# Kernel tuning notes

Measured on AMD Instinct MI355X. Metric: run time of the kernel, lower is better.

## Reference

```python
import jax, jax.numpy as jnp
import numpy as np

B, N, IN_DIM, OUT_DIM = 8, 2048, 128, 128
NEG_SLOPE = 0.2

def setup_inputs() -> dict:
    key = jax.random.key(0)
    k1, k2, k3, k4 = jax.random.split(key, 4)
    x = jax.random.normal(k1, (B, N, IN_DIM), dtype=jnp.float32)
    adj = jax.random.randint(k2, (N, N), 0, 2, dtype=jnp.int32)
    # nn.Linear weight init scale ~ 1/sqrt(fan_in)
    W = jax.random.normal(k3, (IN_DIM, OUT_DIM), dtype=jnp.float32) / np.sqrt(IN_DIM)
    a_vec = jax.random.normal(k4, (2 * OUT_DIM,), dtype=jnp.float32) / np.sqrt(2 * OUT_DIM)
    return {"x": x, "adj": adj, "W": W, "a_vec": a_vec}

def reference(x, adj, W, a_vec):
    # h = x @ W : [b, n, d]
    h = jnp.einsum("bni,io->bno", x, W)
    # Algebraic decomposition of a([h_i, h_j]) = a1.h_i + a2.h_j
    a1, a2 = a_vec[:OUT_DIM], a_vec[OUT_DIM:]
    s_i = h @ a1  # [b, n] score contribution from source node i
    s_j = h @ a2  # [b, n] score contribution from target node j
    e = s_i[:, :, None] + s_j[:, None, :]  # [b, n, n]
    e = jnp.where(e >= 0, e, NEG_SLOPE * e)  # leaky_relu(0.2)
    mask = (adj > 0)[None, :, :]  # [1, n, n] broadcast over batch
    e = jnp.where(mask, e, -jnp.inf)
    alpha = jax.nn.softmax(e, axis=-1)  # [b, n, n]
    out = jnp.einsum("bnm,bmd->bnd", alpha, h)  # [b, n, d]
    return out, alpha
```

## Files before the change

kernel.cpp:

```cpp
#include <hip/hip_runtime.h>
#include <hip/hip_bf16.h>
#include <cstdint>
#include <cstddef>

constexpr int Bn = 8;
constexpr int Nn = 2048;
constexpr int Dn = 128;

typedef __bf16 bf16x8 __attribute__((ext_vector_type(8)));
typedef float f32x4 __attribute__((ext_vector_type(4)));

__global__ __launch_bounds__(256) void gat_k1(
    const float* __restrict__ x, const float* __restrict__ W,
    const float* __restrict__ a_vec,
    __bf16* __restrict__ hT, float* __restrict__ s1, float* __restrict__ s2) {
  __shared__ __align__(16) float Wl[64 * 144];
  __shared__ __align__(16) float xL[32 * 132];

  const int t = threadIdx.x;
  const int r0 = blockIdx.x * 32;
  const int b = r0 >> 11;
  const int n0 = r0 & (Nn - 1);
  const int rp = (t >> 4) << 1;
  const int c0 = (t & 15) << 3;
  const int c0p = c0 + ((c0 >> 5) << 2);

  float acc[2][8];
#pragma unroll
  for (int r = 0; r < 2; ++r)
#pragma unroll
    for (int c = 0; c < 8; ++c) acc[r][c] = 0.f;

#pragma unroll
  for (int it = 0; it < 4; ++it) {
    int idx = t + (it << 8);
    int rr = idx >> 5, kc = (idx & 31) << 2;
    *(float4*)(xL + rr * 132 + kc) = *(const float4*)(x + (size_t)(r0 + rr) * Dn + kc);
  }

  for (int ph = 0; ph < 2; ++ph) {
    if (ph) __syncthreads();
#pragma unroll
    for (int it = 0; it < 8; ++it) {
      int idx = t + (it << 8);
      int kk = idx >> 5, c4 = (idx & 31) << 2;
      int dsto = kk * 144 + c4 + ((c4 >> 5) << 2);
      *(float4*)(Wl + dsto) = *(const float4*)(W + (size_t)((ph << 6) + kk) * Dn + c4);
    }
    __syncthreads();
    const float* xrow = xL + rp * 132 + (ph << 6);
    for (int k = 0; k < 64; ++k) {
      float xa0 = xrow[k];
      float xa1 = xrow[132 + k];
      float4 w0 = *(const float4*)(Wl + k * 144 + c0p);
      float4 w1 = *(const float4*)(Wl + k * 144 + c0p + 4);
      float ws[8] = {w0.x, w0.y, w0.z, w0.w, w1.x, w1.y, w1.z, w1.w};
#pragma unroll
      for (int c = 0; c < 8; ++c) {
        acc[0][c] = fmaf(xa0, ws[c], acc[0][c]);
        acc[1][c] = fmaf(xa1, ws[c], acc[1][c]);
      }
    }
  }

  float q1[2] = {0.f, 0.f}, q2[2] = {0.f, 0.f};
#pragma unroll
  for (int c = 0; c < 8; ++c) {
    float a1c = a_vec[c0 + c];
    float a2c = a_vec[Dn + c0 + c];
    q1[0] = fmaf(acc[0][c], a1c, q1[0]);
    q1[1] = fmaf(acc[1][c], a1c, q1[1]);
    q2[0] = fmaf(acc[0][c], a2c, q2[0]);
    q2[1] = fmaf(acc[1][c], a2c, q2[1]);
  }
#pragma unroll
  for (int d = 1; d < 16; d <<= 1) {
    q1[0] += __shfl_xor(q1[0], d);
    q1[1] += __shfl_xor(q1[1], d);
    q2[0] += __shfl_xor(q2[0], d);
    q2[1] += __shfl_xor(q2[1], d);
  }
  if ((t & 15) == 0) {
    s1[b * Nn + n0 + rp] = q1[0];
    s1[b * Nn + n0 + rp + 1] = q1[1];
    s2[b * Nn + n0 + rp] = q2[0];
    s2[b * Nn + n0 + rp + 1] = q2[1];
  }

#pragma unroll
  for (int c = 0; c < 8; ++c) {
    union { __bf16 h[2]; uint32_t u; } pk;
    pk.h[0] = (__bf16)acc[0][c];
    pk.h[1] = (__bf16)acc[1][c];
    *(uint32_t*)(hT + (size_t)(b * Dn + c0 + c) * Nn + n0 + rp) = pk.u;
  }
}

__global__ __launch_bounds__(512) void gat_k2(
    const int* __restrict__ adj, const __bf16* __restrict__ hT,
    const float* __restrict__ s1, const float* __restrict__ s2,
    float* __restrict__ out, float* __restrict__ alpha) {
  __shared__ __align__(16) float sj[Nn];
  __shared__ float siv[32], invl[32];
  __shared__ __align__(16) __bf16 Pl[2][32 * 72];

  const int t = threadIdx.x;
  const int b = blockIdx.x >> 6;
  const int i0 = (blockIdx.x & 63) << 5;
  const int w = t >> 6, lane = t & 63;
  const int ii = t >> 4, sub = t & 15;
  const int q16 = lane >> 4, m16 = lane & 15;
  const int d0 = w << 4;
  const __bf16* __restrict__ hTb = hT + (size_t)b * Dn * Nn;

  *(float4*)(sj + (t << 2)) = *(const float4*)(s2 + b * Nn + (t << 2));
  if (t < 32) siv[t] = s1[b * Nn + i0 + t];
  __syncthreads();

  const int i = i0 + ii;
  const int* __restrict__ adjrow = adj + (size_t)i * Nn;
  const float si = siv[ii];

  float l = 0.f;
  uint32_t mb0 = 0, mb1 = 0, mb2 = 0, mb3 = 0;
#define PASS1_G(G, MW)                                                        \
  {                                                                           \
    _Pragma("unroll")                                                         \
    for (int u = 0; u < 8; ++u) {                                             \
      int j = (((G) << 3) + u) * 64 + (sub << 2);                             \
      int4 am = *(const int4*)(adjrow + j);                                   \
      float4 sv = *(const float4*)(sj + j);                                   \
      float e0 = si + sv.x; e0 = fmaxf(e0, 0.2f * e0);                        \
      float e1 = si + sv.y; e1 = fmaxf(e1, 0.2f * e1);                        \
      float e2 = si + sv.z; e2 = fmaxf(e2, 0.2f * e2);                        \
      float e3 = si + sv.w; e3 = fmaxf(e3, 0.2f * e3);                        \
      l += (am.x > 0) ? __expf(e0) : 0.f;                                     \
      l += (am.y > 0) ? __expf(e1) : 0.f;                                     \
      l += (am.z > 0) ? __expf(e2) : 0.f;                                     \
      l += (am.w > 0) ? __expf(e3) : 0.f;                                     \
      uint32_t mbt = (am.x > 0 ? 1u : 0u) | (am.y > 0 ? 2u : 0u) |            \
                     (am.z > 0 ? 4u : 0u) | (am.w > 0 ? 8u : 0u);             \
      MW |= mbt << (u << 2);                                                  \
    }                                                                         \
  }
  PASS1_G(0, mb0)
  PASS1_G(1, mb1)
  PASS1_G(2, mb2)
  PASS1_G(3, mb3)
#undef PASS1_G

  l += __shfl_xor(l, 1);
  l += __shfl_xor(l, 2);
  l += __shfl_xor(l, 4);
  l += __shfl_xor(l, 8);
  if (sub == 0) invl[ii] = 1.f / l;
  __syncthreads();
  const float il = invl[ii];

  f32x4 acc0 = {0.f, 0.f, 0.f, 0.f}, acc1 = {0.f, 0.f, 0.f, 0.f};
  float* __restrict__ arow = alpha + ((size_t)(b * Nn + i) << 11);

  const __bf16* __restrict__ bp = hTb + (size_t)(d0 + m16) * Nn + (q16 << 3);

  auto alpha_phase = [&](int k) {
    int j = (k << 6) + (sub << 2);
    float4 sv = *(const float4*)(sj + j);
    uint32_t mw = (k & 16) ? ((k & 8) ? mb3 : mb2) : ((k & 8) ? mb1 : mb0);
    int sh = (k & 7) << 2;
    float e0 = si + sv.x; e0 = fmaxf(e0, 0.2f * e0);
    float e1 = si + sv.y; e1 = fmaxf(e1, 0.2f * e1);
    float e2 = si + sv.z; e2 = fmaxf(e2, 0.2f * e2);
    float e3 = si + sv.w; e3 = fmaxf(e3, 0.2f * e3);
    float a0 = ((mw >> (sh + 0)) & 1u) ? __expf(e0) * il : 0.f;
    float a1 = ((mw >> (sh + 1)) & 1u) ? __expf(e1) * il : 0.f;
    float a2 = ((mw >> (sh + 2)) & 1u) ? __expf(e2) * il : 0.f;
    float a3 = ((mw >> (sh + 3)) & 1u) ? __expf(e3) * il : 0.f;
    f32x4 av = {a0, a1, a2, a3};
    __builtin_nontemporal_store(av, (f32x4*)(arow + j));
    union { __bf16 h[4]; uint2 u2; } pk;
    pk.h[0] = (__bf16)a0; pk.h[1] = (__bf16)a1;
    pk.h[2] = (__bf16)a2; pk.h[3] = (__bf16)a3;
    *(uint2*)(&Pl[k & 1][ii * 72 + (sub << 2)]) = pk.u2;
  };

  auto mfma_win = [&](int k, bf16x8 bc0, bf16x8 bc1) {
    const __bf16* plb = Pl[k & 1];
    bf16x8 a00 = *(const bf16x8*)(plb + m16 * 72 + (q16 << 3));
    bf16x8 a01 = *(const bf16x8*)(plb + m16 * 72 + 32 + (q16 << 3));
    bf16x8 a10 = *(const bf16x8*)(plb + (16 + m16) * 72 + (q16 << 3));
    bf16x8 a11 = *(const bf16x8*)(plb + (16 + m16) * 72 + 32 + (q16 << 3));
    acc0 = __builtin_amdgcn_mfma_f32_16x16x32_bf16(a00, bc0, acc0, 0, 0, 0);
    acc0 = __builtin_amdgcn_mfma_f32_16x16x32_bf16(a01, bc1, acc0, 0, 0, 0);
    acc1 = __builtin_amdgcn_mfma_f32_16x16x32_bf16(a10, bc0, acc1, 0, 0, 0);
    acc1 = __builtin_amdgcn_mfma_f32_16x16x32_bf16(a11, bc1, acc1, 0, 0, 0);
  };

  bf16x8 c0 = *(const bf16x8*)(bp);
  bf16x8 c1 = *(const bf16x8*)(bp + 32);
  alpha_phase(0);
  asm volatile("s_waitcnt lgkmcnt(0)\n\ts_barrier" ::: "memory");

#pragma unroll
  for (int jt = 0; jt < 31; ++jt) {
    bf16x8 n0 = *(const bf16x8*)(bp + ((jt + 1) << 6));
    bf16x8 n1 = *(const bf16x8*)(bp + ((jt + 1) << 6) + 32);
    __builtin_amdgcn_sched_barrier(0);
    mfma_win(jt, c0, c1);
    alpha_phase(jt + 1);
    asm volatile("s_waitcnt lgkmcnt(0)\n\ts_barrier" ::: "memory");
    c0 = n0; c1 = n1;
  }
  mfma_win(31, c0, c1);

#pragma unroll
  for (int ib = 0; ib < 2; ++ib) {
    f32x4 a = ib ? acc1 : acc0;
    int d = d0 + m16;
#pragma unroll
    for (int r = 0; r < 4; ++r) {
      int irow = i0 + (ib << 4) + (q16 << 2) + r;
      out[((size_t)(b * Nn + irow) << 7) + d] = a[r];
    }
  }
}

extern "C" void kernel_launch(void* const* d_in, const int* in_sizes, int n_in,
                              void* d_out, int out_size, void* d_ws, size_t ws_size,
                              hipStream_t stream) {
  const float* x = (const float*)d_in[0];
  const int* adj = (const int*)d_in[1];
  const float* W = (const float*)d_in[2];
  const float* a_vec = (const float*)d_in[3];

  float* out = (float*)d_out;
  float* alpha = out + (size_t)Bn * Nn * Dn;

  char* ws = (char*)d_ws;
  __bf16* hT = (__bf16*)ws;
  float* s1 = (float*)(ws + (size_t)Bn * Dn * Nn * 2);
  float* s2 = s1 + (size_t)Bn * Nn;

  gat_k1<<<512, 256, 0, stream>>>(x, W, a_vec, hT, s1, s2);
  gat_k2<<<512, 512, 0, stream>>>(adj, hT, s1, s2, out, alpha);
}
```

Before: 196.3 us.

## Halve rows per block in GAT attention kernel, widen j-tile, swizzle LDS

The attention kernel now handles 16 query rows per block instead of 32 and launches 1024 blocks, with 32 threads per row covering 128-column tiles over 16 steps instead of 64-column tiles over 32. The P tile in LDS now uses an XOR swizzle in place of padding, each wave issues four MFMAs per tile on a single accumulator, and the launch bounds request higher occupancy. The aim is more blocks in flight and fewer barrier steps to hide memory latency on the large alpha writes. In exchange, the hT B-operand loads are no longer prefetched one tile ahead, and each block reloads the full hT slice for half as many rows, doubling hT reads.

```diff
diff --git a/kernel.cpp b/kernel.cpp
--- a/kernel.cpp
+++ b/kernel.cpp
@@ -96,76 +96,71 @@
   }
 }
 
-__global__ __launch_bounds__(512) void gat_k2(
+__global__ __launch_bounds__(512, 8) void gat_k2(
     const int* __restrict__ adj, const __bf16* __restrict__ hT,
     const float* __restrict__ s1, const float* __restrict__ s2,
     float* __restrict__ out, float* __restrict__ alpha) {
   __shared__ __align__(16) float sj[Nn];
-  __shared__ float siv[32], invl[32];
-  __shared__ __align__(16) __bf16 Pl[2][32 * 72];
+  __shared__ float siv[16], invl[16];
+  __shared__ __align__(16) __bf16 Pl[2][16 * 128];
 
   const int t = threadIdx.x;
-  const int b = blockIdx.x >> 6;
-  const int i0 = (blockIdx.x & 63) << 5;
+  const int b = blockIdx.x >> 7;
+  const int i0 = (blockIdx.x & 127) << 4;
   const int w = t >> 6, lane = t & 63;
-  const int ii = t >> 4, sub = t & 15;
+  const int row = t >> 5;
+  const int jl = (t & 31) << 2;
   const int q16 = lane >> 4, m16 = lane & 15;
   const int d0 = w << 4;
   const __bf16* __restrict__ hTb = hT + (size_t)b * Dn * Nn;
 
   *(float4*)(sj + (t << 2)) = *(const float4*)(s2 + b * Nn + (t << 2));
-  if (t < 32) siv[t] = s1[b * Nn + i0 + t];
+  if (t < 16) siv[t] = s1[b * Nn + i0 + t];
   __syncthreads();
 
-  const int i = i0 + ii;
+  const int i = i0 + row;
   const int* __restrict__ adjrow = adj + (size_t)i * Nn;
-  const float si = siv[ii];
+  const float si = siv[row];
 
   float l = 0.f;
-  uint32_t mb0 = 0, mb1 = 0, mb2 = 0, mb3 = 0;
-#define PASS1_G(G, MW)                                                        \
-  {                                                                           \
-    _Pragma("unroll")                                                         \
-    for (int u = 0; u < 8; ++u) {                                             \
-      int j = (((G) << 3) + u) * 64 + (sub << 2);                             \
-      int4 am = *(const int4*)(adjrow + j);                                   \
-      float4 sv = *(const float4*)(sj + j);                                   \
-      float e0 = si + sv.x; e0 = fmaxf(e0, 0.2f * e0);                        \
-      float e1 = si + sv.y; e1 = fmaxf(e1, 0.2f * e1);                        \
-      float e2 = si + sv.z; e2 = fmaxf(e2, 0.2f * e2);                        \
-      float e3 = si + sv.w; e3 = fmaxf(e3, 0.2f * e3);                        \
-      l += (am.x > 0) ? __expf(e0) : 0.f;                                     \
-      l += (am.y > 0) ? __expf(e1) : 0.f;                                     \
-      l += (am.z > 0) ? __expf(e2) : 0.f;                                     \
-      l += (am.w > 0) ? __expf(e3) : 0.f;                                     \
-      uint32_t mbt = (am.x > 0 ? 1u : 0u) | (am.y > 0 ? 2u : 0u) |            \
-                     (am.z > 0 ? 4u : 0u) | (am.w > 0 ? 8u : 0u);             \
-      MW |= mbt << (u << 2);                                                  \
-    }                                                                         \
-  }
-  PASS1_G(0, mb0)
-  PASS1_G(1, mb1)
-  PASS1_G(2, mb2)
-  PASS1_G(3, mb3)
-#undef PASS1_G
-
+  uint32_t mb0 = 0, mb1 = 0;
+#pragma unroll
+  for (int k = 0; k < 16; ++k) {
+    int j = (k << 7) + jl;
+    int4 am = *(const int4*)(adjrow + j);
+    float4 sv = *(const float4*)(sj + j);
+    float e0 = si + sv.x; e0 = fmaxf(e0, 0.2f * e0);
+    float e1 = si + sv.y; e1 = fmaxf(e1, 0.2f * e1);
+    float e2 = si + sv.z; e2 = fmaxf(e2, 0.2f * e2);
+    float e3 = si + sv.w; e3 = fmaxf(e3, 0.2f * e3);
+    l += (am.x > 0) ? __expf(e0) : 0.f;
+    l += (am.y > 0) ? __expf(e1) : 0.f;
+    l += (am.z > 0) ? __expf(e2) : 0.f;
+    l += (am.w > 0) ? __expf(e3) : 0.f;
+    uint32_t mbt = (am.x > 0 ? 1u : 0u) | (am.y > 0 ? 2u : 0u) |
+                   (am.z > 0 ? 4u : 0u) | (am.w > 0 ? 8u : 0u);
+    if (k < 8) mb0 |= mbt << (k << 2);
+    else       mb1 |= mbt << ((k & 7) << 2);
+  }
   l += __shfl_xor(l, 1);
   l += __shfl_xor(l, 2);
   l += __shfl_xor(l, 4);
   l += __shfl_xor(l, 8);
-  if (sub == 0) invl[ii] = 1.f / l;
+  l += __shfl_xor(l, 16);
+  if ((t & 31) == 0) invl[row] = 1.f / l;
   __syncthreads();
-  const float il = invl[ii];
-
-  f32x4 acc0 = {0.f, 0.f, 0.f, 0.f}, acc1 = {0.f, 0.f, 0.f, 0.f};
+  const float il = invl[row];
+
+  f32x4 acc = {0.f, 0.f, 0.f, 0.f};
   float* __restrict__ arow = alpha + ((size_t)(b * Nn + i) << 11);
 
   const __bf16* __restrict__ bp = hTb + (size_t)(d0 + m16) * Nn + (q16 << 3);
+  const int swz = (m16 & 7) << 4;
 
   auto alpha_phase = [&](int k) {
-    int j = (k << 6) + (sub << 2);
+    int j = (k << 7) + jl;
     float4 sv = *(const float4*)(sj + j);
-    uint32_t mw = (k & 16) ? ((k & 8) ? mb3 : mb2) : ((k & 8) ? mb1 : mb0);
+    uint32_t mw = (k & 8) ? mb1 : mb0;
     int sh = (k & 7) << 2;
     float e0 = si + sv.x; e0 = fmaxf(e0, 0.2f * e0);
     float e1 = si + sv.y; e1 = fmaxf(e1, 0.2f * e1);
@@ -180,47 +175,44 @@
     union { __bf16 h[4]; uint2 u2; } pk;
     pk.h[0] = (__bf16)a0; pk.h[1] = (__bf16)a1;
     pk.h[2] = (__bf16)a2; pk.h[3] = (__bf16)a3;
-    *(uint2*)(&Pl[k & 1][ii * 72 + (sub << 2)]) = pk.u2;
+    *(uint2*)((char*)(&Pl[k & 1][0]) + (row << 8) +
+              (((jl << 1)) ^ ((row & 7) << 4))) = pk.u2;
   };
 
-  auto mfma_win = [&](int k, bf16x8 bc0, bf16x8 bc1) {
-    const __bf16* plb = Pl[k & 1];
-    bf16x8 a00 = *(const bf16x8*)(plb + m16 * 72 + (q16 << 3));
-    bf16x8 a01 = *(const bf16x8*)(plb + m16 * 72 + 32 + (q16 << 3));
-    bf16x8 a10 = *(const bf16x8*)(plb + (16 + m16) * 72 + (q16 << 3));
-    bf16x8 a11 = *(const bf16x8*)(plb + (16 + m16) * 72 + 32 + (q16 << 3));
-    acc0 = __builtin_amdgcn_mfma_f32_16x16x32_bf16(a00, bc0, acc0, 0, 0, 0);
-    acc0 = __builtin_amdgcn_mfma_f32_16x16x32_bf16(a01, bc1, acc0, 0, 0, 0);
-    acc1 = __builtin_amdgcn_mfma_f32_16x16x32_bf16(a10, bc0, acc1, 0, 0, 0);
-    acc1 = __builtin_amdgcn_mfma_f32_16x16x32_bf16(a11, bc1, acc1, 0, 0, 0);
+  auto mfma_win = [&](int parity, bf16x8 c0, bf16x8 c1, bf16x8 c2, bf16x8 c3) {
+    const char* plb = (const char*)(&Pl[parity][0]) + (m16 << 8);
+    bf16x8 a0 = *(const bf16x8*)(plb + (((0 << 6) + (q16 << 4)) ^ swz));
+    bf16x8 a1 = *(const bf16x8*)(plb + (((1 << 6) + (q16 << 4)) ^ swz));
+    bf16x8 a2 = *(const bf16x8*)(plb + (((2 << 6) + (q16 << 4)) ^ swz));
+    bf16x8 a3 = *(const bf16x8*)(plb + (((3 << 6) + (q16 << 4)) ^ swz));
+    acc = __builtin_amdgcn_mfma_f32_16x16x32_bf16(a0, c0, acc, 0, 0, 0);
+    acc = __builtin_amdgcn_mfma_f32_16x16x32_bf16(a1, c1, acc, 0, 0, 0);
+    acc = __builtin_amdgcn_mfma_f32_16x16x32_bf16(a2, c2, acc, 0, 0, 0);
+    acc = __builtin_amdgcn_mfma_f32_16x16x32_bf16(a3, c3, acc, 0, 0, 0);
   };
 
-  bf16x8 c0 = *(const bf16x8*)(bp);
-  bf16x8 c1 = *(const bf16x8*)(bp + 32);
   alpha_phase(0);
   asm volatile("s_waitcnt lgkmcnt(0)\n\ts_barrier" ::: "memory");
 
 #pragma unroll
-  for (int jt = 0; jt < 31; ++jt) {
-    bf16x8 n0 = *(const bf16x8*)(bp + ((jt + 1) << 6));
-    bf16x8 n1 = *(const bf16x8*)(bp + ((jt + 1) << 6) + 32);
+  for (int jt = 0; jt < 16; ++jt) {
+    const __bf16* cp = bp + (jt << 7);
+    bf16x8 c0 = *(const bf16x8*)(cp);
+    bf16x8 c1 = *(const bf16x8*)(cp + 32);
+    bf16x8 c2 = *(const bf16x8*)(cp + 64);
+    bf16x8 c3 = *(const bf16x8*)(cp + 96);
     __builtin_amdgcn_sched_barrier(0);
-    mfma_win(jt, c0, c1);
-    alpha_phase(jt + 1);
-    asm volatile("s_waitcnt lgkmcnt(0)\n\ts_barrier" ::: "memory");
-    c0 = n0; c1 = n1;
-  }
-  mfma_win(31, c0, c1);
-
-#pragma unroll
-  for (int ib = 0; ib < 2; ++ib) {
-    f32x4 a = ib ? acc1 : acc0;
-    int d = d0 + m16;
-#pragma unroll
-    for (int r = 0; r < 4; ++r) {
-      int irow = i0 + (ib << 4) + (q16 << 2) + r;
-      out[((size_t)(b * Nn + irow) << 7) + d] = a[r];
-    }
+    if (jt < 15) alpha_phase(jt + 1);
+    mfma_win(jt & 1, c0, c1, c2, c3);
+    if (jt < 15)
+      asm volatile("s_waitcnt lgkmcnt(0)\n\ts_barrier" ::: "memory");
+  }
+
+  int d = d0 + m16;
+#pragma unroll
+  for (int r = 0; r < 4; ++r) {
+    int irow = i0 + (q16 << 2) + r;
+    out[((size_t)(b * Nn + irow) << 7) + d] = acc[r];
   }
 }
 
@@ -241,5 +233,5 @@
   float* s2 = s1 + (size_t)Bn * Nn;
 
   gat_k1<<<512, 256, 0, stream>>>(x, W, a_vec, hT, s1, s2);
-  gat_k2<<<512, 512, 0, stream>>>(adj, hT, s1, s2, out, alpha);
+  gat_k2<<<1024, 512, 0, stream>>>(adj, hT, s1, s2, out, alpha);
 }
```

Result: slower. 232.0 us (+18.2%).

## Split fused softmax+aggregation kernel into separate alpha and matmul kernels

Applied to the files above, without the earlier changes.

Replaces the fused kernel, which computed alpha and fed it to MFMA through LDS with per-tile barriers, with two kernels. The first computes the masked softmax and writes alpha. The second reads alpha back from global memory as fp32, converts it to bf16 and does the alpha·h matmul with MFMA. This removes the barrier-heavy interleaving and the LDS staging, but adds a full re-read of the 128 MB alpha tensor plus an extra launch.

```diff
diff --git a/kernel.cpp b/kernel.cpp
--- a/kernel.cpp
+++ b/kernel.cpp
@@ -96,30 +96,25 @@
   }
 }
 
-__global__ __launch_bounds__(512) void gat_k2(
-    const int* __restrict__ adj, const __bf16* __restrict__ hT,
-    const float* __restrict__ s1, const float* __restrict__ s2,
-    float* __restrict__ out, float* __restrict__ alpha) {
+__global__ __launch_bounds__(256) void gat_kA(
+    const int* __restrict__ adj, const float* __restrict__ s1,
+    const float* __restrict__ s2, float* __restrict__ alpha) {
   __shared__ __align__(16) float sj[Nn];
-  __shared__ float siv[32], invl[32];
-  __shared__ __align__(16) __bf16 Pl[2][32 * 72];
+  __shared__ float siv[16];
 
   const int t = threadIdx.x;
-  const int b = blockIdx.x >> 6;
-  const int i0 = (blockIdx.x & 63) << 5;
-  const int w = t >> 6, lane = t & 63;
-  const int ii = t >> 4, sub = t & 15;
-  const int q16 = lane >> 4, m16 = lane & 15;
-  const int d0 = w << 4;
-  const __bf16* __restrict__ hTb = hT + (size_t)b * Dn * Nn;
-
-  *(float4*)(sj + (t << 2)) = *(const float4*)(s2 + b * Nn + (t << 2));
-  if (t < 32) siv[t] = s1[b * Nn + i0 + t];
+  const int b = blockIdx.x >> 7;
+  const int i0 = (blockIdx.x & 127) << 4;
+  const int row = t >> 4, sub = t & 15;
+
+  *(float4*)(sj + (t << 3)) = *(const float4*)(s2 + b * Nn + (t << 3));
+  *(float4*)(sj + (t << 3) + 4) = *(const float4*)(s2 + b * Nn + (t << 3) + 4);
+  if (t < 16) siv[t] = s1[b * Nn + i0 + t];
   __syncthreads();
 
-  const int i = i0 + ii;
+  const int i = i0 + row;
   const int* __restrict__ adjrow = adj + (size_t)i * Nn;
-  const float si = siv[ii];
+  const float si = siv[row];
 
   float l = 0.f;
   uint32_t mb0 = 0, mb1 = 0, mb2 = 0, mb3 = 0;
@@ -153,16 +148,12 @@
   l += __shfl_xor(l, 2);
   l += __shfl_xor(l, 4);
   l += __shfl_xor(l, 8);
-  if (sub == 0) invl[ii] = 1.f / l;
-  __syncthreads();
-  const float il = invl[ii];
-
-  f32x4 acc0 = {0.f, 0.f, 0.f, 0.f}, acc1 = {0.f, 0.f, 0.f, 0.f};
+  const float il = 1.f / l;
+
   float* __restrict__ arow = alpha + ((size_t)(b * Nn + i) << 11);
 
-  const __bf16* __restrict__ bp = hTb + (size_t)(d0 + m16) * Nn + (q16 << 3);
-
-  auto alpha_phase = [&](int k) {
+#pragma unroll
+  for (int k = 0; k < 32; ++k) {
     int j = (k << 6) + (sub << 2);
     float4 sv = *(const float4*)(sj + j);
     uint32_t mw = (k & 16) ? ((k & 8) ? mb3 : mb2) : ((k & 8) ? mb1 : mb0);
@@ -177,49 +168,58 @@
     float a3 = ((mw >> (sh + 3)) & 1u) ? __expf(e3) * il : 0.f;
     f32x4 av = {a0, a1, a2, a3};
     __builtin_nontemporal_store(av, (f32x4*)(arow + j));
-    union { __bf16 h[4]; uint2 u2; } pk;
-    pk.h[0] = (__bf16)a0; pk.h[1] = (__bf16)a1;
-    pk.h[2] = (__bf16)a2; pk.h[3] = (__bf16)a3;
-    *(uint2*)(&Pl[k & 1][ii * 72 + (sub << 2)]) = pk.u2;
-  };
-
-  auto mfma_win = [&](int k, bf16x8 bc0, bf16x8 bc1) {
-    const __bf16* plb = Pl[k & 1];
-    bf16x8 a00 = *(const bf16x8*)(plb + m16 * 72 + (q16 << 3));
-    bf16x8 a01 = *(const bf16x8*)(plb + m16 * 72 + 32 + (q16 << 3));
-    bf16x8 a10 = *(const bf16x8*)(plb + (16 + m16) * 72 + (q16 << 3));
-    bf16x8 a11 = *(const bf16x8*)(plb + (16 + m16) * 72 + 32 + (q16 << 3));
-    acc0 = __builtin_amdgcn_mfma_f32_16x16x32_bf16(a00, bc0, acc0, 0, 0, 0);
-    acc0 = __builtin_amdgcn_mfma_f32_16x16x32_bf16(a01, bc1, acc0, 0, 0, 0);
-    acc1 = __builtin_amdgcn_mfma_f32_16x16x32_bf16(a10, bc0, acc1, 0, 0, 0);
-    acc1 = __builtin_amdgcn_mfma_f32_16x16x32_bf16(a11, bc1, acc1, 0, 0, 0);
-  };
-
-  bf16x8 c0 = *(const bf16x8*)(bp);
-  bf16x8 c1 = *(const bf16x8*)(bp + 32);
-  alpha_phase(0);
-  asm volatile("s_waitcnt lgkmcnt(0)\n\ts_barrier" ::: "memory");
-
-#pragma unroll
-  for (int jt = 0; jt < 31; ++jt) {
-    bf16x8 n0 = *(const bf16x8*)(bp + ((jt + 1) << 6));
-    bf16x8 n1 = *(const bf16x8*)(bp + ((jt + 1) << 6) + 32);
-    __builtin_amdgcn_sched_barrier(0);
-    mfma_win(jt, c0, c1);
-    alpha_phase(jt + 1);
-    asm volatile("s_waitcnt lgkmcnt(0)\n\ts_barrier" ::: "memory");
-    c0 = n0; c1 = n1;
-  }
-  mfma_win(31, c0, c1);
-
-#pragma unroll
-  for (int ib = 0; ib < 2; ++ib) {
-    f32x4 a = ib ? acc1 : acc0;
-    int d = d0 + m16;
+  }
+}
+
+__global__ __launch_bounds__(256) void gat_kB(
+    const float* __restrict__ alpha, const __bf16* __restrict__ hT,
+    float* __restrict__ out) {
+  const int t = threadIdx.x;
+  const int b = blockIdx.x >> 6;
+  const int m0 = (blockIdx.x & 63) << 5;
+  const int w = t >> 6, lane = t & 63;
+  const int q16 = lane >> 4, m16 = lane & 15;
+  const int iw = (w & 1) << 4;
+  const int d0w = (w >> 1) << 6;
+
+  const float* __restrict__ arow =
+      alpha + ((size_t)(b * Nn + m0 + iw + m16) << 11) + (q16 << 3);
+  const __bf16* __restrict__ hb = hT + (size_t)b * Dn * Nn + (q16 << 3);
+  const __bf16* __restrict__ hb0 = hb + (size_t)(d0w + 0 * 16 + m16) * Nn;
+  const __bf16* __restrict__ hb1 = hb + (size_t)(d0w + 1 * 16 + m16) * Nn;
+  const __bf16* __restrict__ hb2 = hb + (size_t)(d0w + 2 * 16 + m16) * Nn;
+  const __bf16* __restrict__ hb3 = hb + (size_t)(d0w + 3 * 16 + m16) * Nn;
+
+  f32x4 acc0 = {0.f, 0.f, 0.f, 0.f}, acc1 = {0.f, 0.f, 0.f, 0.f};
+  f32x4 acc2 = {0.f, 0.f, 0.f, 0.f}, acc3 = {0.f, 0.f, 0.f, 0.f};
+
+#pragma unroll 4
+  for (int k0 = 0; k0 < Nn; k0 += 32) {
+    float4 alo = *(const float4*)(arow + k0);
+    float4 ahi = *(const float4*)(arow + k0 + 4);
+    bf16x8 b0 = *(const bf16x8*)(hb0 + k0);
+    bf16x8 b1 = *(const bf16x8*)(hb1 + k0);
+    bf16x8 b2 = *(const bf16x8*)(hb2 + k0);
+    bf16x8 b3 = *(const bf16x8*)(hb3 + k0);
+    bf16x8 af;
+    af[0] = (__bf16)alo.x; af[1] = (__bf16)alo.y;
+    af[2] = (__bf16)alo.z; af[3] = (__bf16)alo.w;
+    af[4] = (__bf16)ahi.x; af[5] = (__bf16)ahi.y;
+    af[6] = (__bf16)ahi.z; af[7] = (__bf16)ahi.w;
+    acc0 = __builtin_amdgcn_mfma_f32_16x16x32_bf16(af, b0, acc0, 0, 0, 0);
+    acc1 = __builtin_amdgcn_mfma_f32_16x16x32_bf16(af, b1, acc1, 0, 0, 0);
+    acc2 = __builtin_amdgcn_mfma_f32_16x16x32_bf16(af, b2, acc2, 0, 0, 0);
+    acc3 = __builtin_amdgcn_mfma_f32_16x16x32_bf16(af, b3, acc3, 0, 0, 0);
+  }
+
+  const int ibase = m0 + iw + (q16 << 2);
+#pragma unroll
+  for (int dt = 0; dt < 4; ++dt) {
+    f32x4 a = (dt == 0) ? acc0 : (dt == 1) ? acc1 : (dt == 2) ? acc2 : acc3;
+    int d = d0w + (dt << 4) + m16;
 #pragma unroll
     for (int r = 0; r < 4; ++r) {
-      int irow = i0 + (ib << 4) + (q16 << 2) + r;
-      out[((size_t)(b * Nn + irow) << 7) + d] = a[r];
+      out[((size_t)(b * Nn + ibase + r) << 7) + d] = a[r];
     }
   }
 }
@@ -241,5 +241,6 @@
   float* s2 = s1 + (size_t)Bn * Nn;
 
   gat_k1<<<512, 256, 0, stream>>>(x, W, a_vec, hT, s1, s2);
-  gat_k2<<<512, 512, 0, stream>>>(adj, hT, s1, s2, out, alpha);
-}
+  gat_kA<<<1024, 256, 0, stream>>>(adj, s1, s2, alpha);
+  gat_kB<<<512, 256, 0, stream>>>(alpha, hT, out);
+}
```

New measurement: 297.1 us. 51.4% more time.
